# Kernel tuning notes

Measured on AMD Instinct MI355X. Metric: run time of the kernel, lower is better.

Reference implementation:

```python
import jax, jax.numpy as jnp
import numpy as np

DIM = 384
NUM_HEADS = 12
WS = 8            # window_size
SS = 4            # shift_size
HEAD_DIM = DIM // NUM_HEADS
SCALE = HEAD_DIM ** -0.5
N = WS * WS       # tokens per window
EPS = 1e-5
MLP_HIDDEN = 4 * DIM

# relative position index (static, matches torch buffer construction)
_coords = np.stack(np.meshgrid(np.arange(WS), np.arange(WS), indexing='ij')).reshape(2, -1)
_rel = (_coords[:, :, None] - _coords[:, None, :]).transpose(1, 2, 0)  # [N,N,2]
_rel[..., 0] += WS - 1
_rel[..., 1] += WS - 1
_rel[..., 0] *= 2 * WS - 1
RPI = jnp.asarray(_rel.sum(-1))  # [N,N] int


def layer_norm(x, g, b):
    m = x.mean(-1, keepdims=True)
    v = ((x - m) ** 2).mean(-1, keepdims=True)
    return (x - m) / jnp.sqrt(v + EPS) * g + b


def window_partition(x):
    B, Hh, Ww, C = x.shape
    x = x.reshape(B, Hh // WS, WS, Ww // WS, WS, C).transpose(0, 1, 3, 2, 4, 5)
    return x.reshape(-1, WS, WS, C)


def window_reverse(w, Hh, Ww):
    B = w.shape[0] // ((Hh // WS) * (Ww // WS))
    x = w.reshape(B, Hh // WS, Ww // WS, WS, WS, -1).transpose(0, 1, 3, 2, 4, 5)
    return x.reshape(B, Hh, Ww, -1)


def attention_mask(Hp, Wp):
    # region id along each axis: 0 = [0, Hp-WS), 1 = [Hp-WS, Hp-SS), 2 = [Hp-SS, Hp)
    h_id = np.zeros(Hp, np.int32); h_id[Hp - WS:Hp - SS] = 1; h_id[Hp - SS:] = 2
    w_id = np.zeros(Wp, np.int32); w_id[Wp - WS:Wp - SS] = 1; w_id[Wp - SS:] = 2
    cnt = h_id[:, None] * 3 + w_id[None, :]                      # [Hp, Wp]
    img = jnp.asarray(cnt, jnp.float32).reshape(1, Hp, Wp, 1)
    mw = window_partition(img).reshape(-1, N)                    # [nW, N]
    am = mw[:, None, :] - mw[:, :, None]                         # [nW, N, N]
    return jnp.where(am != 0, jnp.float32(-100.0), jnp.float32(0.0))


def setup_inputs() -> dict:
    key = jax.random.key(0)
    ks = jax.random.split(key, 8)
    B, H, W = 32, 64, 64
    std = 0.02
    return {
        'x': jax.random.normal(ks[0], (B, H * W, DIM), jnp.float32),
        'qkv_w': jax.random.normal(ks[1], (DIM, 3 * DIM), jnp.float32) * std,
        'qkv_b': jnp.zeros((3 * DIM,), jnp.float32),
        'proj_w': jax.random.normal(ks[2], (DIM, DIM), jnp.float32) * std,
        'proj_b': jnp.zeros((DIM,), jnp.float32),
        'rpb_table': jax.random.normal(ks[3], ((2 * WS - 1) * (2 * WS - 1), NUM_HEADS), jnp.float32) * std,
        'n1_g': jnp.ones((DIM,), jnp.float32), 'n1_b': jnp.zeros((DIM,), jnp.float32),
        'n2_g': jnp.ones((DIM,), jnp.float32), 'n2_b': jnp.zeros((DIM,), jnp.float32),
        'fc1_w': jax.random.normal(ks[4], (DIM, MLP_HIDDEN), jnp.float32) * std,
        'fc1_b': jnp.zeros((MLP_HIDDEN,), jnp.float32),
        'fc2_w': jax.random.normal(ks[5], (MLP_HIDDEN, DIM), jnp.float32) * std,
        'fc2_b': jnp.zeros((DIM,), jnp.float32),
        'H': 64, 'W': 64,
    }


def reference(x, qkv_w, qkv_b, proj_w, proj_b, rpb_table, n1_g, n1_b, n2_g, n2_b,
              fc1_w, fc1_b, fc2_w, fc2_b, H, W):
    B, L, C = x.shape
    shortcut = x
    h = layer_norm(x, n1_g, n1_b).reshape(B, H, W, C)
    pad_r = (WS - W % WS) % WS
    pad_b = (WS - H % WS) % WS
    if pad_r or pad_b:
        h = jnp.pad(h, ((0, 0), (0, pad_b), (0, pad_r), (0, 0)))
    Hp, Wp = H + pad_b, W + pad_r
    shifted = jnp.roll(h, shift=(-SS, -SS), axis=(1, 2))
    xw = window_partition(shifted).reshape(-1, N, C)             # [B_, N, C]
    B_ = xw.shape[0]

    qkv = (xw @ qkv_w + qkv_b).reshape(B_, N, 3, NUM_HEADS, HEAD_DIM)
    q = qkv[:, :, 0].transpose(0, 2, 1, 3) * SCALE               # [B_, h, N, d]
    k = qkv[:, :, 1].transpose(0, 2, 1, 3)
    v = qkv[:, :, 2].transpose(0, 2, 1, 3)

    attn = jnp.einsum('bhnd,bhmd->bhnm', q, k)                   # [B_, h, N, N]
    bias = rpb_table[RPI].transpose(2, 0, 1)                     # [h, N, N]
    attn = attn + bias[None]

    mask = attention_mask(Hp, Wp)                                # [nW, N, N]
    nW = mask.shape[0]
    attn = attn.reshape(B_ // nW, nW, NUM_HEADS, N, N) + mask[None, :, None]
    attn = jax.nn.softmax(attn.reshape(B_, NUM_HEADS, N, N), axis=-1)

    out = jnp.einsum('bhnm,bhmd->bhnd', attn, v)
    out = out.transpose(0, 2, 1, 3).reshape(B_, N, C)
    out = out @ proj_w + proj_b

    out = window_reverse(out.reshape(-1, WS, WS, C), Hp, Wp)
    out = jnp.roll(out, shift=(SS, SS), axis=(1, 2))
    out = out[:, :H, :W, :].reshape(B, H * W, C)

    x = shortcut + out
    h2 = layer_norm(x, n2_g, n2_b)
    mlp = jax.nn.gelu(h2 @ fc1_w + fc1_b, approximate=False) @ fc2_w + fc2_b
    return x + mlp
```

## Files before the change

kernel.cpp:

```cpp
#include <hip/hip_runtime.h>
#include <math.h>


#define ROWS_TOTAL 131072
#define NWIN_TOTAL 2048

typedef __attribute__((ext_vector_type(8))) __bf16 bf16x8;
typedef __attribute__((ext_vector_type(4))) float f32x4;
typedef __attribute__((ext_vector_type(8))) unsigned short ushort8;

__device__ __forceinline__ unsigned short f2bf(float f) {
  unsigned u = __builtin_bit_cast(unsigned, f);
  u = (u + 0x7fffu + ((u >> 16) & 1u)) >> 16;
  return (unsigned short)u;
}

__device__ __forceinline__ void gload16(const void* g, void* l) {
  __builtin_amdgcn_global_load_lds(
      (const __attribute__((address_space(1))) unsigned int*)g,
      (__attribute__((address_space(3))) unsigned int*)l, 16, 0, 0);
}

__device__ __forceinline__ int gather_row(int win, int t) {
  int b = win >> 6, wi = (win >> 3) & 7, wj = win & 7;
  int gi = (wi * 8 + (t >> 3) + 4) & 63;
  int gj = (wj * 8 + (t & 7) + 4) & 63;
  return (b << 12) + (gi << 6) + gj;
}

__device__ __forceinline__ void frag_mma(const ushort* As_, const ushort* Bs_,
                                         int wr, int wc, int lane,
                                         f32x4 acc[4][4]) {
  const int go = (((lane >> 4) ^ ((lane >> 1) & 3)) << 3);
  const int lr = lane & 15;
  bf16x8 af[4], bfr[4];
#pragma unroll
  for (int mi = 0; mi < 4; ++mi)
    af[mi] = *(const bf16x8*)(As_ + (wr * 64 + mi * 16 + lr) * 32 + go);
#pragma unroll
  for (int nj = 0; nj < 4; ++nj)
    bfr[nj] = *(const bf16x8*)(Bs_ + (wc * 64 + nj * 16 + lr) * 32 + go);
#pragma unroll
  for (int mi = 0; mi < 4; ++mi)
#pragma unroll
    for (int nj = 0; nj < 4; ++nj)
      acc[mi][nj] = __builtin_amdgcn_mfma_f32_16x16x32_bf16(
          af[mi], bfr[nj], acc[mi][nj], 0, 0, 0);
}

#define VM4() asm volatile("s_waitcnt vmcnt(4)" ::: "memory")
#define VM0() asm volatile("s_waitcnt vmcnt(0)" ::: "memory")
#define SCB() __builtin_amdgcn_sched_barrier(0)
#define BARR() __builtin_amdgcn_s_barrier()

#define STG(B_, T_)                                   \
  { size_t ko = (size_t)(T_) * 64;                    \
    gload16(aS0 + ko, &As[B_][w * 1024]);             \
    gload16(aS1 + ko, &As[B_][w * 1024 + 512]);       \
    gload16(bS0 + ko, &Bs[B_][w * 1024]);             \
    gload16(bS1 + ko, &Bs[B_][w * 1024 + 512]); }

#define GEMM_PIPE(NK)                                               \
  {                                                                 \
    STG(0, 0);                                                      \
    STG(1, 1);                                                      \
    VM4(); SCB(); BARR(); SCB();                                    \
    int cur = 0;                                                    \
    for (int t = 0; t < (NK); ++t) {                                \
      if (t + 2 < (NK)) {                                           \
        int nb = cur + 2; if (nb >= 3) nb -= 3;                     \
        STG(nb, t + 2);                                             \
      }                                                             \
      __builtin_amdgcn_s_setprio(1);                                \
      frag_mma(&As[cur][0], &Bs[cur][0], wr, wc, lane, acc);        \
      __builtin_amdgcn_s_setprio(0);                                \
      if (t + 2 < (NK)) { VM4(); } else { VM0(); }                  \
      SCB(); BARR(); SCB();                                         \
      ++cur; if (cur == 3) cur = 0;                                 \
    }                                                               \
  }

__global__ __launch_bounds__(256) void wprep_k(
    const float* __restrict__ qkvw, const float* __restrict__ projw,
    const float* __restrict__ fc1w, const float* __restrict__ fc2w,
    ushort* __restrict__ wq, ushort* __restrict__ wp,
    ushort* __restrict__ w1, ushort* __restrict__ w2) {
  int gid = blockIdx.x * 256 + threadIdx.x;
  const int S1 = 1152 * 384;
  const int S2 = S1 + 384 * 384;
  const int S3 = S2 + 1536 * 384;
  const int S4 = S3 + 384 * 1536;
  if (gid < S1) {
    int n = gid / 384, k = gid - n * 384;
    wq[gid] = f2bf(qkvw[(size_t)k * 1152 + n]);
  } else if (gid < S2) {
    int i = gid - S1, n = i / 384, k = i - n * 384;
    wp[i] = f2bf(projw[(size_t)k * 384 + n]);
  } else if (gid < S3) {
    int i = gid - S2, n = i / 384, k = i - n * 384;
    w1[i] = f2bf(fc1w[(size_t)k * 1536 + n]);
  } else if (gid < S4) {
    int i = gid - S3, n = i / 1536, k = i - n * 1536;
    w2[i] = f2bf(fc2w[(size_t)k * 384 + n]);
  }
}

__global__ void ln_stats_k(const float* __restrict__ x, float* __restrict__ st) {
  int wid = threadIdx.x >> 6, lane = threadIdx.x & 63;
  int row = (blockIdx.x << 2) + wid;
  const float* p = x + (size_t)row * 384;
  float s = 0.f, ss = 0.f;
#pragma unroll
  for (int c = 0; c < 3; ++c) {
    float2 v = *(const float2*)(p + lane * 2 + c * 128);
    s += v.x + v.y;
    ss += v.x * v.x + v.y * v.y;
  }
#pragma unroll
  for (int o = 32; o > 0; o >>= 1) {
    s += __shfl_down(s, o);
    ss += __shfl_down(ss, o);
  }
  if (lane == 0) {
    float m = s * (1.f / 384.f);
    float var = ss * (1.f / 384.f) - m * m;
    *(float2*)(st + (size_t)row * 2) = make_float2(m, rsqrtf(var + 1e-5f));
  }
}

__global__ __launch_bounds__(256) void ln_apply_k(
    const float* __restrict__ x, const float* __restrict__ st,
    const float* __restrict__ g, const float* __restrict__ b,
    ushort* __restrict__ o) {
  int gid = blockIdx.x * 256 + threadIdx.x;
  int row = gid / 48, c8 = (gid - row * 48) * 8;
  float2 s2 = *(const float2*)(st + (size_t)row * 2);
  const float* xp = x + (size_t)row * 384 + c8;
  float4 v0 = *(const float4*)xp, v1 = *(const float4*)(xp + 4);
  float4 g0 = *(const float4*)(g + c8), g1 = *(const float4*)(g + c8 + 4);
  float4 b0 = *(const float4*)(b + c8), b1 = *(const float4*)(b + c8 + 4);
  float m = s2.x, r = s2.y;
  ushort8 w;
  w[0] = f2bf((v0.x - m) * r * g0.x + b0.x);
  w[1] = f2bf((v0.y - m) * r * g0.y + b0.y);
  w[2] = f2bf((v0.z - m) * r * g0.z + b0.z);
  w[3] = f2bf((v0.w - m) * r * g0.w + b0.w);
  w[4] = f2bf((v1.x - m) * r * g1.x + b1.x);
  w[5] = f2bf((v1.y - m) * r * g1.y + b1.y);
  w[6] = f2bf((v1.z - m) * r * g1.z + b1.z);
  w[7] = f2bf((v1.w - m) * r * g1.w + b1.w);
  *(ushort8*)(o + (size_t)row * 384 + c8) = w;
}

__global__ __launch_bounds__(256) void qkv_mfma_k(
    const ushort* __restrict__ xln, const ushort* __restrict__ wq,
    const float* __restrict__ qkvb, float* __restrict__ qd,
    float* __restrict__ kd, float* __restrict__ vd, int wc0) {
  __shared__ __align__(16) ushort As[3][4096];
  __shared__ __align__(16) ushort Bs[3][4096];
  __shared__ int rowS[128];
  const int tid = threadIdx.x;
  const int w = tid >> 6, lane = tid & 63;
  const int wr = w >> 1, wc = w & 1;
  const int bm = blockIdx.x, n0 = blockIdx.y * 128;
  if (tid < 128) {
    int win = wc0 + bm * 2 + (tid >> 6);
    rowS[tid] = gather_row(win, tid & 63);
  }
  __syncthreads();
  const int rA = w * 32 + (lane >> 2);
  const int sle = (((lane & 3) ^ ((lane >> 3) & 3)) << 4);
  const char* aS0 = (const char*)xln + (size_t)rowS[rA] * 768 + sle;
  const char* aS1 = (const char*)xln + (size_t)rowS[rA + 16] * 768 + sle;
  const char* bS0 = (const char*)wq + (size_t)(n0 + rA) * 768 + sle;
  const char* bS1 = (const char*)wq + (size_t)(n0 + rA + 16) * 768 + sle;
  f32x4 acc[4][4];
#pragma unroll
  for (int i = 0; i < 4; ++i)
#pragma unroll
    for (int j = 0; j < 4; ++j) acc[i][j] = (f32x4)(0.f);
  GEMM_PIPE(12);
  const float scale = 0.17677669529663687f;
#pragma unroll
  for (int mi = 0; mi < 4; ++mi) {
#pragma unroll
    for (int r = 0; r < 4; ++r) {
      int rr = wr * 64 + mi * 16 + ((lane >> 4) << 2) + r;
      int w_rel = bm * 2 + (rr >> 6), t = rr & 63;
#pragma unroll
      for (int nj = 0; nj < 4; ++nj) {
        int nc = n0 + wc * 64 + nj * 16 + (lane & 15);
        float v = acc[mi][nj][r] + qkvb[nc];
        int qi = nc / 384, rem = nc - qi * 384;
        int hh = rem >> 5, d = rem & 31;
        float* base = (qi == 0) ? qd : (qi == 1 ? kd : vd);
        if (qi == 0) v *= scale;
        base[(((size_t)w_rel * 12 + hh) << 11) + (t << 5) + d] = v;
      }
    }
  }
}

__global__ __launch_bounds__(128) void attn_k(
    const float* __restrict__ q, const float* __restrict__ k,
    const float* __restrict__ v, const float* __restrict__ rpb,
    ushort* __restrict__ ao, int wc0) {
  __shared__ __align__(16) float kbuf[2][64][32];
  __shared__ __align__(16) float vbuf[2][64][32];
  __shared__ float bias[2][232];
  __shared__ int region[64];
  const int tid = threadIdx.x;
  const int wid = tid >> 6, lane = tid & 63;
  const int w = blockIdx.x, win = wc0 + w;
  const int head = blockIdx.y * 2 + wid;
  if (tid < 64) {
    int wi = (win >> 3) & 7, wj = win & 7;
    int pi = wi * 8 + (tid >> 3), pj = wj * 8 + (tid & 7);
    int ri = pi < 56 ? 0 : (pi < 60 ? 1 : 2);
    int rj = pj < 56 ? 0 : (pj < 60 ? 1 : 2);
    region[tid] = ri * 3 + rj;
  }
  const size_t hb = ((size_t)w * 12 + head) * 2048;
  const float* kp = k + hb;
  const float* vp = v + hb;
#pragma unroll
  for (int s = 0; s < 8; ++s) {
    int f = s * 64 + lane;
    int r = f >> 3, c = (f & 7) << 2;
    *(float4*)&kbuf[wid][r][c] = *(const float4*)(kp + r * 32 + c);
    *(float4*)&vbuf[wid][r][c] = *(const float4*)(vp + r * 32 + c);
  }
  for (int s = lane; s < 225; s += 64) bias[wid][s] = rpb[s * 12 + head];
  __syncthreads();
  const int i = lane;
  float qr[32];
  const float* qp = q + hb + (i << 5);
#pragma unroll
  for (int c = 0; c < 32; c += 4) {
    float4 t4 = *(const float4*)(qp + c);
    qr[c] = t4.x; qr[c + 1] = t4.y; qr[c + 2] = t4.z; qr[c + 3] = t4.w;
  }
  const int yi = i >> 3, xi = i & 7, regi = region[i];
  float sc[64];
  float mx = -3.0e38f;
#pragma unroll
  for (int j = 0; j < 64; ++j) {
    float a = 0.f;
#pragma unroll
    for (int c = 0; c < 32; c += 4) {
      float4 kv = *(float4*)&kbuf[wid][j][c];
      a = fmaf(qr[c], kv.x, a);
      a = fmaf(qr[c + 1], kv.y, a);
      a = fmaf(qr[c + 2], kv.z, a);
      a = fmaf(qr[c + 3], kv.w, a);
    }
    int dy = yi - (j >> 3) + 7, dx = xi - (j & 7) + 7;
    a += bias[wid][dy * 15 + dx];
    if (region[j] != regi) a -= 100.f;
    sc[j] = a;
    mx = fmaxf(mx, a);
  }
  float sum = 0.f;
#pragma unroll
  for (int j = 0; j < 64; ++j) {
    float e = __expf(sc[j] - mx);
    sc[j] = e;
    sum += e;
  }
  const float inv = 1.f / sum;
  float o[32];
#pragma unroll
  for (int c = 0; c < 32; ++c) o[c] = 0.f;
#pragma unroll
  for (int j = 0; j < 64; ++j) {
    float p = sc[j];
#pragma unroll
    for (int c = 0; c < 32; c += 4) {
      float4 vv = *(float4*)&vbuf[wid][j][c];
      o[c] = fmaf(p, vv.x, o[c]);
      o[c + 1] = fmaf(p, vv.y, o[c + 1]);
      o[c + 2] = fmaf(p, vv.z, o[c + 2]);
      o[c + 3] = fmaf(p, vv.w, o[c + 3]);
    }
  }
  ushort* op = ao + ((size_t)(w * 64 + i)) * 384 + (head << 5);
#pragma unroll
  for (int c = 0; c < 32; c += 8) {
    ushort8 pk;
#pragma unroll
    for (int j2 = 0; j2 < 8; ++j2) pk[j2] = f2bf(o[c + j2] * inv);
    *(ushort8*)(op + c) = pk;
  }
}

__global__ __launch_bounds__(256) void proj_mfma_k(
    const ushort* __restrict__ ao, const ushort* __restrict__ wp,
    const float* __restrict__ pb, const float* __restrict__ x,
    float* __restrict__ x2, int wc0) {
  __shared__ __align__(16) ushort As[3][4096];
  __shared__ __align__(16) ushort Bs[3][4096];
  const int tid = threadIdx.x;
  const int w = tid >> 6, lane = tid & 63;
  const int wr = w >> 1, wc = w & 1;
  const int bm = blockIdx.x, n0 = blockIdx.y * 128;
  const int rA = w * 32 + (lane >> 2);
  const int sle = (((lane & 3) ^ ((lane >> 3) & 3)) << 4);
  const char* aS0 = (const char*)ao + (size_t)(bm * 128 + rA) * 768 + sle;
  const char* aS1 = aS0 + (size_t)16 * 768;
  const char* bS0 = (const char*)wp + (size_t)(n0 + rA) * 768 + sle;
  const char* bS1 = bS0 + (size_t)16 * 768;
  f32x4 acc[4][4];
#pragma unroll
  for (int i = 0; i < 4; ++i)
#pragma unroll
    for (int j = 0; j < 4; ++j) acc[i][j] = (f32x4)(0.f);
  GEMM_PIPE(12);
#pragma unroll
  for (int mi = 0; mi < 4; ++mi) {
#pragma unroll
    for (int r = 0; r < 4; ++r) {
      int rr = wr * 64 + mi * 16 + ((lane >> 4) << 2) + r;
      int lw = (bm * 128 + rr) >> 6, t = rr & 63;
      int gr = gather_row(wc0 + lw, t);
#pragma unroll
      for (int nj = 0; nj < 4; ++nj) {
        int nc = n0 + wc * 64 + nj * 16 + (lane & 15);
        size_t idx = (size_t)gr * 384 + nc;
        x2[idx] = acc[mi][nj][r] + pb[nc] + x[idx];
      }
    }
  }
}

__global__ __launch_bounds__(256) void fc1_mfma_k(
    const ushort* __restrict__ x2ln, const ushort* __restrict__ w1,
    const float* __restrict__ fb, ushort* __restrict__ hm, int row0) {
  __shared__ __align__(16) ushort As[3][4096];
  __shared__ __align__(16) ushort Bs[3][4096];
  const int tid = threadIdx.x;
  const int w = tid >> 6, lane = tid & 63;
  const int wr = w >> 1, wc = w & 1;
  const int bm = blockIdx.x, n0 = blockIdx.y * 128;
  const int rA = w * 32 + (lane >> 2);
  const int sle = (((lane & 3) ^ ((lane >> 3) & 3)) << 4);
  const char* aS0 =
      (const char*)x2ln + (size_t)(row0 + bm * 128 + rA) * 768 + sle;
  const char* aS1 = aS0 + (size_t)16 * 768;
  const char* bS0 = (const char*)w1 + (size_t)(n0 + rA) * 768 + sle;
  const char* bS1 = bS0 + (size_t)16 * 768;
  f32x4 acc[4][4];
#pragma unroll
  for (int i = 0; i < 4; ++i)
#pragma unroll
    for (int j = 0; j < 4; ++j) acc[i][j] = (f32x4)(0.f);
  GEMM_PIPE(12);
#pragma unroll
  for (int mi = 0; mi < 4; ++mi) {
#pragma unroll
    for (int r = 0; r < 4; ++r) {
      int rr = wr * 64 + mi * 16 + ((lane >> 4) << 2) + r;
      size_t lrow = (size_t)(bm * 128 + rr);
#pragma unroll
      for (int nj = 0; nj < 4; ++nj) {
        int nc = n0 + wc * 64 + nj * 16 + (lane & 15);
        float v = acc[mi][nj][r] + fb[nc];
        v = 0.5f * v * (1.f + erff(v * 0.70710678118654752f));
        hm[lrow * 1536 + nc] = f2bf(v);
      }
    }
  }
}

__global__ __launch_bounds__(256) void fc2_mfma_k(
    const ushort* __restrict__ hm, const ushort* __restrict__ w2,
    const float* __restrict__ fb, float* __restrict__ out, int row0) {
  __shared__ __align__(16) ushort As[3][4096];
  __shared__ __align__(16) ushort Bs[3][4096];
  const int tid = threadIdx.x;
  const int w = tid >> 6, lane = tid & 63;
  const int wr = w >> 1, wc = w & 1;
  const int bm = blockIdx.x, n0 = blockIdx.y * 128;
  const int rA = w * 32 + (lane >> 2);
  const int sle = (((lane & 3) ^ ((lane >> 3) & 3)) << 4);
  const char* aS0 = (const char*)hm + (size_t)(bm * 128 + rA) * 3072 + sle;
  const char* aS1 = aS0 + (size_t)16 * 3072;
  const char* bS0 = (const char*)w2 + (size_t)(n0 + rA) * 3072 + sle;
  const char* bS1 = bS0 + (size_t)16 * 3072;
  f32x4 acc[4][4];
#pragma unroll
  for (int i = 0; i < 4; ++i)
#pragma unroll
    for (int j = 0; j < 4; ++j) acc[i][j] = (f32x4)(0.f);
  GEMM_PIPE(48);
#pragma unroll
  for (int mi = 0; mi < 4; ++mi) {
#pragma unroll
    for (int r = 0; r < 4; ++r) {
      int rr = wr * 64 + mi * 16 + ((lane >> 4) << 2) + r;
      size_t grow = (size_t)(row0 + bm * 128 + rr);
#pragma unroll
      for (int nj = 0; nj < 4; ++nj) {
        int nc = n0 + wc * 64 + nj * 16 + (lane & 15);
        size_t idx = grow * 384 + nc;
        out[idx] = out[idx] + acc[mi][nj][r] + fb[nc];
      }
    }
  }
}

extern "C" void kernel_launch(void* const* d_in, const int* in_sizes, int n_in,
                              void* d_out, int out_size, void* d_ws, size_t ws_size,
                              hipStream_t stream) {
  const float* x = (const float*)d_in[0];
  const float* qkv_w = (const float*)d_in[1];
  const float* qkv_b = (const float*)d_in[2];
  const float* proj_w = (const float*)d_in[3];
  const float* proj_b = (const float*)d_in[4];
  const float* rpb = (const float*)d_in[5];
  const float* n1g = (const float*)d_in[6];
  const float* n1b = (const float*)d_in[7];
  const float* n2g = (const float*)d_in[8];
  const float* n2b = (const float*)d_in[9];
  const float* fc1w = (const float*)d_in[10];
  const float* fc1b = (const float*)d_in[11];
  const float* fc2w = (const float*)d_in[12];
  const float* fc2b = (const float*)d_in[13];
  float* out = (float*)d_out;
  char* ws = (char*)d_ws;

  float* st1 = (float*)ws;
  float* st2 = (float*)(ws + 1048576);
  ushort* wq = (ushort*)(ws + 2097152);
  ushort* wp = wq + 442368;
  ushort* w1 = wp + 147456;
  ushort* w2 = w1 + 589824;
  ushort* xln = (ushort*)(ws + 5636096);
  char* scratch = ws + 5636096 + 100663296;
  size_t base = 5636096 + 100663296;
  size_t ssz = (ws_size > base) ? ws_size - base : 0;

  wprep_k<<<6912, 256, 0, stream>>>(qkv_w, proj_w, fc1w, fc2w, wq, wp, w1, w2);
  ln_stats_k<<<ROWS_TOTAL / 4, 256, 0, stream>>>(x, st1);
  ln_apply_k<<<ROWS_TOTAL * 48 / 256, 256, 0, stream>>>(x, st1, n1g, n1b, xln);

  const size_t perwin = 344064;
  int nwc = (int)(ssz / perwin);
  if (nwc > NWIN_TOTAL) nwc = NWIN_TOTAL;
  nwc &= ~1;
  if (nwc < 2) nwc = 2;
  float* qd = (float*)scratch;
  float* kd = qd + (size_t)nwc * 24576;
  float* vd = kd + (size_t)nwc * 24576;
  ushort* ao = (ushort*)(vd + (size_t)nwc * 24576);
  for (int wc0 = 0; wc0 < NWIN_TOTAL; wc0 += nwc) {
    int nw = (NWIN_TOTAL - wc0 < nwc) ? (NWIN_TOTAL - wc0) : nwc;
    qkv_mfma_k<<<dim3(nw / 2, 9), 256, 0, stream>>>(xln, wq, qkv_b, qd, kd, vd, wc0);
    attn_k<<<dim3(nw, 6), 128, 0, stream>>>(qd, kd, vd, rpb, ao, wc0);
    proj_mfma_k<<<dim3(nw / 2, 3), 256, 0, stream>>>(ao, wp, proj_b, x, out, wc0);
  }

  ln_stats_k<<<ROWS_TOTAL / 4, 256, 0, stream>>>(out, st2);
  ln_apply_k<<<ROWS_TOTAL * 48 / 256, 256, 0, stream>>>(out, st2, n2g, n2b, xln);
  const size_t pergrp = 393216;
  int ngc = (int)(ssz / pergrp);
  if (ngc > 1024) ngc = 1024;
  if (ngc < 1) ngc = 1;
  ushort* hm = (ushort*)scratch;
  for (int g0 = 0; g0 < 1024; g0 += ngc) {
    int ng = (1024 - g0 < ngc) ? (1024 - g0) : ngc;
    fc1_mfma_k<<<dim3(ng, 12), 256, 0, stream>>>(xln, w1, fc1b, hm, g0 * 128);
    fc2_mfma_k<<<dim3(ng, 3), 256, 0, stream>>>(hm, w2, fc2b, out, g0 * 128);
  }
}
```

Before: 1.574 ms.

## Enlarge GEMM M-tile to 256 rows and fuse LayerNorm stats with apply

All four MFMA GEMM kernels go from 128x128 to 256x128 block tiles, so each wave computes 128x64 with 8x4 accumulators and the B tile is reused across twice as many rows. The load staging, wait counts, grid sizes and chunk loops are updated to match, and launch_bounds(256,2) is added. The separate LayerNorm stats and apply kernels are merged into one kernel that keeps each row in registers, which removes a second read of the activations and the stats buffer. The larger tile raises register and LDS use (about 72KB per block), which may lower occupancy, and it halves the number of blocks per launch.

```diff
diff --git a/kernel.cpp b/kernel.cpp
--- a/kernel.cpp
+++ b/kernel.cpp
@@ -30,41 +30,42 @@
 
 __device__ __forceinline__ void frag_mma(const ushort* As_, const ushort* Bs_,
                                          int wr, int wc, int lane,
-                                         f32x4 acc[4][4]) {
+                                         f32x4 acc[8][4]) {
   const int go = (((lane >> 4) ^ ((lane >> 1) & 3)) << 3);
   const int lr = lane & 15;
-  bf16x8 af[4], bfr[4];
-#pragma unroll
-  for (int mi = 0; mi < 4; ++mi)
-    af[mi] = *(const bf16x8*)(As_ + (wr * 64 + mi * 16 + lr) * 32 + go);
+  bf16x8 bfr[4];
 #pragma unroll
   for (int nj = 0; nj < 4; ++nj)
     bfr[nj] = *(const bf16x8*)(Bs_ + (wc * 64 + nj * 16 + lr) * 32 + go);
 #pragma unroll
-  for (int mi = 0; mi < 4; ++mi)
+  for (int mi = 0; mi < 8; ++mi) {
+    bf16x8 af = *(const bf16x8*)(As_ + (wr * 128 + mi * 16 + lr) * 32 + go);
 #pragma unroll
     for (int nj = 0; nj < 4; ++nj)
       acc[mi][nj] = __builtin_amdgcn_mfma_f32_16x16x32_bf16(
-          af[mi], bfr[nj], acc[mi][nj], 0, 0, 0);
-}
-
-#define VM4() asm volatile("s_waitcnt vmcnt(4)" ::: "memory")
+          af, bfr[nj], acc[mi][nj], 0, 0, 0);
+  }
+}
+
+#define VM6() asm volatile("s_waitcnt vmcnt(6)" ::: "memory")
 #define VM0() asm volatile("s_waitcnt vmcnt(0)" ::: "memory")
 #define SCB() __builtin_amdgcn_sched_barrier(0)
 #define BARR() __builtin_amdgcn_s_barrier()
 
-#define STG(B_, T_)                                   \
-  { size_t ko = (size_t)(T_) * 64;                    \
-    gload16(aS0 + ko, &As[B_][w * 1024]);             \
-    gload16(aS1 + ko, &As[B_][w * 1024 + 512]);       \
-    gload16(bS0 + ko, &Bs[B_][w * 1024]);             \
-    gload16(bS1 + ko, &Bs[B_][w * 1024 + 512]); }
+#define STG(B_, T_)                                    \
+  { size_t ko = (size_t)(T_) * 64;                     \
+    gload16(aS0 + ko, &As[B_][aD]);                    \
+    gload16(aS1 + ko, &As[B_][aD + 512]);              \
+    gload16(aS2 + ko, &As[B_][aD + 1024]);             \
+    gload16(aS3 + ko, &As[B_][aD + 1536]);             \
+    gload16(bS0 + ko, &Bs[B_][bD]);                    \
+    gload16(bS1 + ko, &Bs[B_][bD + 512]); }
 
 #define GEMM_PIPE(NK)                                               \
   {                                                                 \
     STG(0, 0);                                                      \
     STG(1, 1);                                                      \
-    VM4(); SCB(); BARR(); SCB();                                    \
+    VM6(); SCB(); BARR(); SCB();                                    \
     int cur = 0;                                                    \
     for (int t = 0; t < (NK); ++t) {                                \
       if (t + 2 < (NK)) {                                           \
@@ -74,7 +75,7 @@
       __builtin_amdgcn_s_setprio(1);                                \
       frag_mma(&As[cur][0], &Bs[cur][0], wr, wc, lane, acc);        \
       __builtin_amdgcn_s_setprio(0);                                \
-      if (t + 2 < (NK)) { VM4(); } else { VM0(); }                  \
+      if (t + 2 < (NK)) { VM6(); } else { VM0(); }                  \
       SCB(); BARR(); SCB();                                         \
       ++cur; if (cur == 3) cur = 0;                                 \
     }                                                               \
@@ -105,88 +106,79 @@
   }
 }
 
-__global__ void ln_stats_k(const float* __restrict__ x, float* __restrict__ st) {
+__global__ __launch_bounds__(256) void ln_fused_k(
+    const float* __restrict__ x, const float* __restrict__ g,
+    const float* __restrict__ b, ushort* __restrict__ o) {
   int wid = threadIdx.x >> 6, lane = threadIdx.x & 63;
   int row = (blockIdx.x << 2) + wid;
   const float* p = x + (size_t)row * 384;
+  float2 v[3];
   float s = 0.f, ss = 0.f;
 #pragma unroll
   for (int c = 0; c < 3; ++c) {
-    float2 v = *(const float2*)(p + lane * 2 + c * 128);
-    s += v.x + v.y;
-    ss += v.x * v.x + v.y * v.y;
-  }
-#pragma unroll
-  for (int o = 32; o > 0; o >>= 1) {
-    s += __shfl_down(s, o);
-    ss += __shfl_down(ss, o);
-  }
-  if (lane == 0) {
-    float m = s * (1.f / 384.f);
-    float var = ss * (1.f / 384.f) - m * m;
-    *(float2*)(st + (size_t)row * 2) = make_float2(m, rsqrtf(var + 1e-5f));
-  }
-}
-
-__global__ __launch_bounds__(256) void ln_apply_k(
-    const float* __restrict__ x, const float* __restrict__ st,
-    const float* __restrict__ g, const float* __restrict__ b,
-    ushort* __restrict__ o) {
-  int gid = blockIdx.x * 256 + threadIdx.x;
-  int row = gid / 48, c8 = (gid - row * 48) * 8;
-  float2 s2 = *(const float2*)(st + (size_t)row * 2);
-  const float* xp = x + (size_t)row * 384 + c8;
-  float4 v0 = *(const float4*)xp, v1 = *(const float4*)(xp + 4);
-  float4 g0 = *(const float4*)(g + c8), g1 = *(const float4*)(g + c8 + 4);
-  float4 b0 = *(const float4*)(b + c8), b1 = *(const float4*)(b + c8 + 4);
-  float m = s2.x, r = s2.y;
-  ushort8 w;
-  w[0] = f2bf((v0.x - m) * r * g0.x + b0.x);
-  w[1] = f2bf((v0.y - m) * r * g0.y + b0.y);
-  w[2] = f2bf((v0.z - m) * r * g0.z + b0.z);
-  w[3] = f2bf((v0.w - m) * r * g0.w + b0.w);
-  w[4] = f2bf((v1.x - m) * r * g1.x + b1.x);
-  w[5] = f2bf((v1.y - m) * r * g1.y + b1.y);
-  w[6] = f2bf((v1.z - m) * r * g1.z + b1.z);
-  w[7] = f2bf((v1.w - m) * r * g1.w + b1.w);
-  *(ushort8*)(o + (size_t)row * 384 + c8) = w;
-}
-
-__global__ __launch_bounds__(256) void qkv_mfma_k(
+    v[c] = *(const float2*)(p + lane * 2 + c * 128);
+    s += v[c].x + v[c].y;
+    ss += v[c].x * v[c].x + v[c].y * v[c].y;
+  }
+#pragma unroll
+  for (int off = 1; off < 64; off <<= 1) {
+    s += __shfl_xor(s, off);
+    ss += __shfl_xor(ss, off);
+  }
+  float m = s * (1.f / 384.f);
+  float r = rsqrtf(ss * (1.f / 384.f) - m * m + 1e-5f);
+  ushort* op = o + (size_t)row * 384;
+#pragma unroll
+  for (int c = 0; c < 3; ++c) {
+    float2 gg = *(const float2*)(g + lane * 2 + c * 128);
+    float2 bb = *(const float2*)(b + lane * 2 + c * 128);
+    union { ushort u[2]; unsigned w; } pk;
+    pk.u[0] = f2bf((v[c].x - m) * r * gg.x + bb.x);
+    pk.u[1] = f2bf((v[c].y - m) * r * gg.y + bb.y);
+    *(unsigned*)(op + lane * 2 + c * 128) = pk.w;
+  }
+}
+
+__global__ __launch_bounds__(256, 2) void qkv_mfma_k(
     const ushort* __restrict__ xln, const ushort* __restrict__ wq,
     const float* __restrict__ qkvb, float* __restrict__ qd,
     float* __restrict__ kd, float* __restrict__ vd, int wc0) {
-  __shared__ __align__(16) ushort As[3][4096];
+  __shared__ __align__(16) ushort As[3][8192];
   __shared__ __align__(16) ushort Bs[3][4096];
-  __shared__ int rowS[128];
+  __shared__ int rowS[256];
   const int tid = threadIdx.x;
   const int w = tid >> 6, lane = tid & 63;
   const int wr = w >> 1, wc = w & 1;
   const int bm = blockIdx.x, n0 = blockIdx.y * 128;
-  if (tid < 128) {
-    int win = wc0 + bm * 2 + (tid >> 6);
+  {
+    int win = wc0 + bm * 4 + (tid >> 6);
     rowS[tid] = gather_row(win, tid & 63);
   }
   __syncthreads();
-  const int rA = w * 32 + (lane >> 2);
   const int sle = (((lane & 3) ^ ((lane >> 3) & 3)) << 4);
-  const char* aS0 = (const char*)xln + (size_t)rowS[rA] * 768 + sle;
-  const char* aS1 = (const char*)xln + (size_t)rowS[rA + 16] * 768 + sle;
-  const char* bS0 = (const char*)wq + (size_t)(n0 + rA) * 768 + sle;
-  const char* bS1 = (const char*)wq + (size_t)(n0 + rA + 16) * 768 + sle;
-  f32x4 acc[4][4];
-#pragma unroll
-  for (int i = 0; i < 4; ++i)
+  const int rb = w * 64 + (lane >> 2);
+  const char* aS0 = (const char*)xln + (size_t)rowS[rb] * 768 + sle;
+  const char* aS1 = (const char*)xln + (size_t)rowS[rb + 16] * 768 + sle;
+  const char* aS2 = (const char*)xln + (size_t)rowS[rb + 32] * 768 + sle;
+  const char* aS3 = (const char*)xln + (size_t)rowS[rb + 48] * 768 + sle;
+  const int nb = n0 + w * 32 + (lane >> 2);
+  const char* bS0 = (const char*)wq + (size_t)nb * 768 + sle;
+  const char* bS1 = (const char*)wq + (size_t)(nb + 16) * 768 + sle;
+  const int aD = w * 2048 + lane * 8;
+  const int bD = w * 1024 + lane * 8;
+  f32x4 acc[8][4];
+#pragma unroll
+  for (int i = 0; i < 8; ++i)
 #pragma unroll
     for (int j = 0; j < 4; ++j) acc[i][j] = (f32x4)(0.f);
   GEMM_PIPE(12);
   const float scale = 0.17677669529663687f;
 #pragma unroll
-  for (int mi = 0; mi < 4; ++mi) {
+  for (int mi = 0; mi < 8; ++mi) {
 #pragma unroll
     for (int r = 0; r < 4; ++r) {
-      int rr = wr * 64 + mi * 16 + ((lane >> 4) << 2) + r;
-      int w_rel = bm * 2 + (rr >> 6), t = rr & 63;
+      int rr = wr * 128 + mi * 16 + ((lane >> 4) << 2) + r;
+      int w_rel = bm * 4 + (rr >> 6), t = rr & 63;
 #pragma unroll
       for (int nj = 0; nj < 4; ++nj) {
         int nc = n0 + wc * 64 + nj * 16 + (lane & 15);
@@ -293,35 +285,40 @@
   }
 }
 
-__global__ __launch_bounds__(256) void proj_mfma_k(
+__global__ __launch_bounds__(256, 2) void proj_mfma_k(
     const ushort* __restrict__ ao, const ushort* __restrict__ wp,
     const float* __restrict__ pb, const float* __restrict__ x,
     float* __restrict__ x2, int wc0) {
-  __shared__ __align__(16) ushort As[3][4096];
+  __shared__ __align__(16) ushort As[3][8192];
   __shared__ __align__(16) ushort Bs[3][4096];
   const int tid = threadIdx.x;
   const int w = tid >> 6, lane = tid & 63;
   const int wr = w >> 1, wc = w & 1;
   const int bm = blockIdx.x, n0 = blockIdx.y * 128;
-  const int rA = w * 32 + (lane >> 2);
   const int sle = (((lane & 3) ^ ((lane >> 3) & 3)) << 4);
-  const char* aS0 = (const char*)ao + (size_t)(bm * 128 + rA) * 768 + sle;
+  const int rb = bm * 256 + w * 64 + (lane >> 2);
+  const char* aS0 = (const char*)ao + (size_t)rb * 768 + sle;
   const char* aS1 = aS0 + (size_t)16 * 768;
-  const char* bS0 = (const char*)wp + (size_t)(n0 + rA) * 768 + sle;
-  const char* bS1 = bS0 + (size_t)16 * 768;
-  f32x4 acc[4][4];
-#pragma unroll
-  for (int i = 0; i < 4; ++i)
+  const char* aS2 = aS0 + (size_t)32 * 768;
+  const char* aS3 = aS0 + (size_t)48 * 768;
+  const int nb = n0 + w * 32 + (lane >> 2);
+  const char* bS0 = (const char*)wp + (size_t)nb * 768 + sle;
+  const char* bS1 = (const char*)wp + (size_t)(nb + 16) * 768 + sle;
+  const int aD = w * 2048 + lane * 8;
+  const int bD = w * 1024 + lane * 8;
+  f32x4 acc[8][4];
+#pragma unroll
+  for (int i = 0; i < 8; ++i)
 #pragma unroll
     for (int j = 0; j < 4; ++j) acc[i][j] = (f32x4)(0.f);
   GEMM_PIPE(12);
 #pragma unroll
-  for (int mi = 0; mi < 4; ++mi) {
+  for (int mi = 0; mi < 8; ++mi) {
 #pragma unroll
     for (int r = 0; r < 4; ++r) {
-      int rr = wr * 64 + mi * 16 + ((lane >> 4) << 2) + r;
-      int lw = (bm * 128 + rr) >> 6, t = rr & 63;
-      int gr = gather_row(wc0 + lw, t);
+      int rr = wr * 128 + mi * 16 + ((lane >> 4) << 2) + r;
+      int gl = bm * 256 + rr;
+      int gr = gather_row(wc0 + (gl >> 6), gl & 63);
 #pragma unroll
       for (int nj = 0; nj < 4; ++nj) {
         int nc = n0 + wc * 64 + nj * 16 + (lane & 15);
@@ -332,34 +329,38 @@
   }
 }
 
-__global__ __launch_bounds__(256) void fc1_mfma_k(
+__global__ __launch_bounds__(256, 2) void fc1_mfma_k(
     const ushort* __restrict__ x2ln, const ushort* __restrict__ w1,
     const float* __restrict__ fb, ushort* __restrict__ hm, int row0) {
-  __shared__ __align__(16) ushort As[3][4096];
+  __shared__ __align__(16) ushort As[3][8192];
   __shared__ __align__(16) ushort Bs[3][4096];
   const int tid = threadIdx.x;
   const int w = tid >> 6, lane = tid & 63;
   const int wr = w >> 1, wc = w & 1;
   const int bm = blockIdx.x, n0 = blockIdx.y * 128;
-  const int rA = w * 32 + (lane >> 2);
   const int sle = (((lane & 3) ^ ((lane >> 3) & 3)) << 4);
-  const char* aS0 =
-      (const char*)x2ln + (size_t)(row0 + bm * 128 + rA) * 768 + sle;
+  const int rb = row0 + bm * 256 + w * 64 + (lane >> 2);
+  const char* aS0 = (const char*)x2ln + (size_t)rb * 768 + sle;
   const char* aS1 = aS0 + (size_t)16 * 768;
-  const char* bS0 = (const char*)w1 + (size_t)(n0 + rA) * 768 + sle;
-  const char* bS1 = bS0 + (size_t)16 * 768;
-  f32x4 acc[4][4];
-#pragma unroll
-  for (int i = 0; i < 4; ++i)
+  const char* aS2 = aS0 + (size_t)32 * 768;
+  const char* aS3 = aS0 + (size_t)48 * 768;
+  const int nb = n0 + w * 32 + (lane >> 2);
+  const char* bS0 = (const char*)w1 + (size_t)nb * 768 + sle;
+  const char* bS1 = (const char*)w1 + (size_t)(nb + 16) * 768 + sle;
+  const int aD = w * 2048 + lane * 8;
+  const int bD = w * 1024 + lane * 8;
+  f32x4 acc[8][4];
+#pragma unroll
+  for (int i = 0; i < 8; ++i)
 #pragma unroll
     for (int j = 0; j < 4; ++j) acc[i][j] = (f32x4)(0.f);
   GEMM_PIPE(12);
 #pragma unroll
-  for (int mi = 0; mi < 4; ++mi) {
+  for (int mi = 0; mi < 8; ++mi) {
 #pragma unroll
     for (int r = 0; r < 4; ++r) {
-      int rr = wr * 64 + mi * 16 + ((lane >> 4) << 2) + r;
-      size_t lrow = (size_t)(bm * 128 + rr);
+      int rr = wr * 128 + mi * 16 + ((lane >> 4) << 2) + r;
+      size_t lrow = (size_t)(bm * 256 + rr);
 #pragma unroll
       for (int nj = 0; nj < 4; ++nj) {
         int nc = n0 + wc * 64 + nj * 16 + (lane & 15);
@@ -371,33 +372,38 @@
   }
 }
 
-__global__ __launch_bounds__(256) void fc2_mfma_k(
+__global__ __launch_bounds__(256, 2) void fc2_mfma_k(
     const ushort* __restrict__ hm, const ushort* __restrict__ w2,
     const float* __restrict__ fb, float* __restrict__ out, int row0) {
-  __shared__ __align__(16) ushort As[3][4096];
+  __shared__ __align__(16) ushort As[3][8192];
   __shared__ __align__(16) ushort Bs[3][4096];
   const int tid = threadIdx.x;
   const int w = tid >> 6, lane = tid & 63;
   const int wr = w >> 1, wc = w & 1;
   const int bm = blockIdx.x, n0 = blockIdx.y * 128;
-  const int rA = w * 32 + (lane >> 2);
   const int sle = (((lane & 3) ^ ((lane >> 3) & 3)) << 4);
-  const char* aS0 = (const char*)hm + (size_t)(bm * 128 + rA) * 3072 + sle;
+  const int rb = bm * 256 + w * 64 + (lane >> 2);
+  const char* aS0 = (const char*)hm + (size_t)rb * 3072 + sle;
   const char* aS1 = aS0 + (size_t)16 * 3072;
-  const char* bS0 = (const char*)w2 + (size_t)(n0 + rA) * 3072 + sle;
-  const char* bS1 = bS0 + (size_t)16 * 3072;
-  f32x4 acc[4][4];
-#pragma unroll
-  for (int i = 0; i < 4; ++i)
+  const char* aS2 = aS0 + (size_t)32 * 3072;
+  const char* aS3 = aS0 + (size_t)48 * 3072;
+  const int nb = n0 + w * 32 + (lane >> 2);
+  const char* bS0 = (const char*)w2 + (size_t)nb * 3072 + sle;
+  const char* bS1 = (const char*)w2 + (size_t)(nb + 16) * 3072 + sle;
+  const int aD = w * 2048 + lane * 8;
+  const int bD = w * 1024 + lane * 8;
+  f32x4 acc[8][4];
+#pragma unroll
+  for (int i = 0; i < 8; ++i)
 #pragma unroll
     for (int j = 0; j < 4; ++j) acc[i][j] = (f32x4)(0.f);
   GEMM_PIPE(48);
 #pragma unroll
-  for (int mi = 0; mi < 4; ++mi) {
+  for (int mi = 0; mi < 8; ++mi) {
 #pragma unroll
     for (int r = 0; r < 4; ++r) {
-      int rr = wr * 64 + mi * 16 + ((lane >> 4) << 2) + r;
-      size_t grow = (size_t)(row0 + bm * 128 + rr);
+      int rr = wr * 128 + mi * 16 + ((lane >> 4) << 2) + r;
+      size_t grow = (size_t)(row0 + bm * 256 + rr);
 #pragma unroll
       for (int nj = 0; nj < 4; ++nj) {
         int nc = n0 + wc * 64 + nj * 16 + (lane & 15);
@@ -428,47 +434,43 @@
   float* out = (float*)d_out;
   char* ws = (char*)d_ws;
 
-  float* st1 = (float*)ws;
-  float* st2 = (float*)(ws + 1048576);
-  ushort* wq = (ushort*)(ws + 2097152);
+  ushort* wq = (ushort*)ws;
   ushort* wp = wq + 442368;
   ushort* w1 = wp + 147456;
   ushort* w2 = w1 + 589824;
-  ushort* xln = (ushort*)(ws + 5636096);
-  char* scratch = ws + 5636096 + 100663296;
-  size_t base = 5636096 + 100663296;
+  ushort* xln = (ushort*)(ws + 3538944);
+  char* scratch = ws + 3538944 + 100663296;
+  size_t base = 3538944 + 100663296;
   size_t ssz = (ws_size > base) ? ws_size - base : 0;
 
   wprep_k<<<6912, 256, 0, stream>>>(qkv_w, proj_w, fc1w, fc2w, wq, wp, w1, w2);
-  ln_stats_k<<<ROWS_TOTAL / 4, 256, 0, stream>>>(x, st1);
-  ln_apply_k<<<ROWS_TOTAL * 48 / 256, 256, 0, stream>>>(x, st1, n1g, n1b, xln);
+  ln_fused_k<<<ROWS_TOTAL / 4, 256, 0, stream>>>(x, n1g, n1b, xln);
 
   const size_t perwin = 344064;
   int nwc = (int)(ssz / perwin);
   if (nwc > NWIN_TOTAL) nwc = NWIN_TOTAL;
-  nwc &= ~1;
-  if (nwc < 2) nwc = 2;
+  nwc &= ~3;
+  if (nwc < 4) nwc = 4;
   float* qd = (float*)scratch;
   float* kd = qd + (size_t)nwc * 24576;
   float* vd = kd + (size_t)nwc * 24576;
   ushort* ao = (ushort*)(vd + (size_t)nwc * 24576);
   for (int wc0 = 0; wc0 < NWIN_TOTAL; wc0 += nwc) {
     int nw = (NWIN_TOTAL - wc0 < nwc) ? (NWIN_TOTAL - wc0) : nwc;
-    qkv_mfma_k<<<dim3(nw / 2, 9), 256, 0, stream>>>(xln, wq, qkv_b, qd, kd, vd, wc0);
+    qkv_mfma_k<<<dim3(nw / 4, 9), 256, 0, stream>>>(xln, wq, qkv_b, qd, kd, vd, wc0);
     attn_k<<<dim3(nw, 6), 128, 0, stream>>>(qd, kd, vd, rpb, ao, wc0);
-    proj_mfma_k<<<dim3(nw / 2, 3), 256, 0, stream>>>(ao, wp, proj_b, x, out, wc0);
-  }
-
-  ln_stats_k<<<ROWS_TOTAL / 4, 256, 0, stream>>>(out, st2);
-  ln_apply_k<<<ROWS_TOTAL * 48 / 256, 256, 0, stream>>>(out, st2, n2g, n2b, xln);
-  const size_t pergrp = 393216;
+    proj_mfma_k<<<dim3(nw / 4, 3), 256, 0, stream>>>(ao, wp, proj_b, x, out, wc0);
+  }
+
+  ln_fused_k<<<ROWS_TOTAL / 4, 256, 0, stream>>>(out, n2g, n2b, xln);
+  const size_t pergrp = 786432;
   int ngc = (int)(ssz / pergrp);
-  if (ngc > 1024) ngc = 1024;
+  if (ngc > 512) ngc = 512;
   if (ngc < 1) ngc = 1;
   ushort* hm = (ushort*)scratch;
-  for (int g0 = 0; g0 < 1024; g0 += ngc) {
-    int ng = (1024 - g0 < ngc) ? (1024 - g0) : ngc;
-    fc1_mfma_k<<<dim3(ng, 12), 256, 0, stream>>>(xln, w1, fc1b, hm, g0 * 128);
-    fc2_mfma_k<<<dim3(ng, 3), 256, 0, stream>>>(hm, w2, fc2b, out, g0 * 128);
-  }
-}
+  for (int g0 = 0; g0 < 512; g0 += ngc) {
+    int ng = (512 - g0 < ngc) ? (512 - g0) : ngc;
+    fc1_mfma_k<<<dim3(ng, 12), 256, 0, stream>>>(xln, w1, fc1b, hm, g0 * 256);
+    fc2_mfma_k<<<dim3(ng, 3), 256, 0, stream>>>(hm, w2, fc2b, out, g0 * 256);
+  }
+}
```

Measured after the change: 1.600 ms. About the same (+1.7%).
